# Optimization experiments

Hardware: AMD Instinct MI355X
Metric: run time of the kernel (lower is better)

## Reference

```python
import jax, jax.numpy as jnp
import numpy as np

N_NODES = 50000
NUM_FEATS = 512
HIDDEN = 128
NUM_LAYERS = 4
NUM_CLASSES = 40
N_EDGES = 800000
ALPHA = 0.1
C_MIN = 0.2
RESIDUAL_WEIGHT = C_MIN - ALPHA  # 0.1
BIAS_SRELU = -10.0


def setup_inputs() -> dict:
    key = jax.random.key(0)
    ks = jax.random.split(key, 8)
    x = jax.random.normal(ks[0], (N_NODES, NUM_FEATS), dtype=jnp.float32)
    edge_index = jax.random.randint(ks[1], (2, N_EDGES), 0, N_NODES, dtype=jnp.int64)
    W_in = jax.random.normal(ks[2], (NUM_FEATS, HIDDEN), dtype=jnp.float32) / np.sqrt(NUM_FEATS)
    b_in = jnp.zeros((HIDDEN,), dtype=jnp.float32)
    W_layers = jax.random.normal(ks[3], (NUM_LAYERS, HIDDEN, HIDDEN), dtype=jnp.float32) / np.sqrt(HIDDEN)
    srelu_bias = jnp.full((NUM_LAYERS, HIDDEN), BIAS_SRELU, dtype=jnp.float32)
    W_out = jax.random.normal(ks[4], (HIDDEN, NUM_CLASSES), dtype=jnp.float32) / np.sqrt(HIDDEN)
    b_out = jnp.zeros((NUM_CLASSES,), dtype=jnp.float32)
    return {"x": x, "edge_index": edge_index, "W_in": W_in, "b_in": b_in,
            "W_layers": W_layers, "srelu_bias": srelu_bias,
            "W_out": W_out, "b_out": b_out}


def _gcn_norm(edge_index, n):
    # PyG gcn_norm: add self-loops, symmetric normalization D^-1/2 A D^-1/2
    loop = jnp.arange(n, dtype=edge_index.dtype)
    src = jnp.concatenate([edge_index[0], loop])
    dst = jnp.concatenate([edge_index[1], loop])
    ones = jnp.ones(src.shape[0], dtype=jnp.float32)
    deg = jax.ops.segment_sum(ones, dst, num_segments=n)
    dinv = jnp.where(deg > 0, jax.lax.rsqrt(deg), 0.0)
    norm = dinv[src] * dinv[dst]  # [E+N]
    return src, dst, norm


def reference(x, edge_index, W_in, b_in, W_layers, srelu_bias, W_out, b_out):
    n = x.shape[0]
    src, dst, norm = _gcn_norm(edge_index, n)

    # input layer (eval mode: dropout is identity), non-arxiv path
    h = jax.nn.relu(x @ W_in + b_in)
    x0 = h  # original_x residual anchor

    def layer(h, params):
        W, sb = params
        # sparse gather-scale-scatter aggregation: [E, H] messages
        agg = jax.ops.segment_sum(norm[:, None] * h[src], dst, num_segments=n)
        out = (1.0 - ALPHA - RESIDUAL_WEIGHT) * agg + RESIDUAL_WEIGHT * h + ALPHA * x0
        out = out @ W
        out = jax.nn.relu(out - sb) + sb  # SReLU
        return out, None

    h, _ = jax.lax.scan(layer, h, (W_layers, srelu_bias))
    return h @ W_out + b_out
```

## Files before the change

kernel.cpp:

```cpp
#include <hip/hip_runtime.h>
#include <hip/hip_fp16.h>

#define N_NODES 50000
#define E_EDGES 800000
#define F_IN 512
#define HID 128
#define N_LAYERS 4
#define C_OUT 40
#define SCAN_BLOCKS 196

typedef __attribute__((ext_vector_type(8))) short bf16x8;
typedef __attribute__((ext_vector_type(4))) float f32x4;

#define MFMA16(a, b, c) __builtin_amdgcn_mfma_f32_16x16x32_bf16(a, b, c, 0, 0, 0)

__device__ __forceinline__ void split2(float a, unsigned short& hi, unsigned short& lo) {
    unsigned u = __float_as_uint(a);
    unsigned r = u + 0x7FFFu + ((u >> 16) & 1u);
    hi = (unsigned short)(r >> 16);
    float hf = __uint_as_float(((unsigned)hi) << 16);
    lo = (unsigned short)(__float_as_uint(a - hf) >> 16);
}

__device__ __forceinline__ void async16(void* lds, const void* g) {
    __builtin_amdgcn_global_load_lds(
        (const __attribute__((address_space(1))) unsigned*)g,
        (__attribute__((address_space(3))) unsigned*)lds, 16, 0, 0);
}

__global__ void indeg_count(const int* __restrict__ ei, int* __restrict__ indeg) {
    int e = blockIdx.x * 256 + threadIdx.x;
    if (e < E_EDGES) {
        unsigned d = (unsigned)ei[E_EDGES + e];
        if (d < N_NODES) atomicAdd(&indeg[d], 1);
    }
}

__global__ void scan_p1(const int* __restrict__ indeg, int* __restrict__ bsum,
                        float* __restrict__ dinv) {
    __shared__ int red[4];
    int i = blockIdx.x * 256 + threadIdx.x;
    int v = (i < N_NODES) ? indeg[i] : 0;
    if (i < N_NODES) dinv[i] = rsqrtf(1.0f + (float)v);
    int s = v;
    #pragma unroll
    for (int off = 32; off > 0; off >>= 1) s += __shfl_down(s, off, 64);
    if ((threadIdx.x & 63) == 0) red[threadIdx.x >> 6] = s;
    __syncthreads();
    if (threadIdx.x == 0) bsum[blockIdx.x] = red[0] + red[1] + red[2] + red[3];
}

__launch_bounds__(256)
__global__ void scan_p2(const int* __restrict__ bsum, int* __restrict__ boff,
                        int* __restrict__ rowptr) {
    __shared__ int s[256];
    int t = threadIdx.x;
    int v = (t < SCAN_BLOCKS) ? bsum[t] : 0;
    s[t] = v;
    __syncthreads();
    #pragma unroll
    for (int off = 1; off < 256; off <<= 1) {
        int a = s[t];
        int b = (t >= off) ? s[t - off] : 0;
        __syncthreads();
        s[t] = a + b;
        __syncthreads();
    }
    if (t < SCAN_BLOCKS) boff[t] = (t == 0) ? 0 : s[t - 1];
    if (t == 255) rowptr[N_NODES] = s[SCAN_BLOCKS - 1];
}

__launch_bounds__(256)
__global__ void scan_p3(const int* __restrict__ indeg, const int* __restrict__ boff,
                        int* __restrict__ rowptr, int* __restrict__ cursor) {
    __shared__ int s[256];
    int t = threadIdx.x;
    int i = blockIdx.x * 256 + t;
    int v = (i < N_NODES) ? indeg[i] : 0;
    s[t] = v;
    __syncthreads();
    #pragma unroll
    for (int off = 1; off < 256; off <<= 1) {
        int a = s[t];
        int b = (t >= off) ? s[t - off] : 0;
        __syncthreads();
        s[t] = a + b;
        __syncthreads();
    }
    if (i < N_NODES) {
        int excl = boff[blockIdx.x] + s[t] - v;
        rowptr[i] = excl;
        cursor[i] = excl;
    }
}

__global__ void csr_fill(const int* __restrict__ ei, int* __restrict__ cursor,
                         int* __restrict__ csr) {
    int e = blockIdx.x * 256 + threadIdx.x;
    if (e < E_EDGES) {
        unsigned s = (unsigned)ei[e];
        unsigned d = (unsigned)ei[E_EDGES + e];
        if (s < N_NODES && d < N_NODES) {
            int pos = atomicAdd(&cursor[d], 1);
            csr[pos] = (int)s;
        }
    }
}

__global__ void wprep(const float* __restrict__ Wi, const float* __restrict__ Wl,
                      const float* __restrict__ Wo,
                      unsigned short* __restrict__ Wth, unsigned short* __restrict__ Wtl,
                      unsigned short* __restrict__ Wlth, unsigned short* __restrict__ Wltl,
                      unsigned short* __restrict__ Woth, unsigned short* __restrict__ Wotl) {
    int idx = blockIdx.x * 256 + threadIdx.x;
    unsigned short hi, lo;
    if (idx < F_IN * HID) {
        int k = idx >> 7, n = idx & 127;
        split2(Wi[idx], hi, lo);
        Wth[(size_t)n * F_IN + k] = hi;
        Wtl[(size_t)n * F_IN + k] = lo;
    } else if (idx < 2 * F_IN * HID) {
        int j = idx - F_IN * HID;
        int l = j >> 14, rem = j & 16383;
        int k = rem >> 7, n = rem & 127;
        split2(Wl[j], hi, lo);
        Wlth[(size_t)l * HID * HID + n * HID + k] = hi;
        Wltl[(size_t)l * HID * HID + n * HID + k] = lo;
    } else if (idx < 2 * F_IN * HID + 48 * HID) {
        int j = idx - 2 * F_IN * HID;
        int n = j >> 7, k = j & 127;
        float w = (n < C_OUT) ? Wo[(size_t)k * C_OUT + n] : 0.f;
        split2(w, hi, lo);
        Woth[(size_t)n * HID + k] = hi;
        Wotl[(size_t)n * HID + k] = lo;
    }
}

__launch_bounds__(256)
__global__ void gemm_in_mfma(const float* __restrict__ x,
                             const unsigned short* __restrict__ Bth,
                             const unsigned short* __restrict__ Btl,
                             const float* __restrict__ bi,
                             const float* __restrict__ dinv,
                             float* __restrict__ x0out,
                             __half* __restrict__ g16) {
    __shared__ __align__(16) unsigned short Ah[64 * 32];
    __shared__ __align__(16) unsigned short Al[64 * 32];
    __shared__ __align__(16) unsigned short Bh[2][128 * 32];
    __shared__ __align__(16) unsigned short Bl[2][128 * 32];
    const int t = threadIdx.x;
    const int lane = t & 63;
    const int wv = t >> 6;
    const int wr = wv >> 1, wc = wv & 1;
    const int row0 = blockIdx.x * 64;
    const int fr = lane & 15;
    const int fkg = lane >> 4;
    const float4 z4 = make_float4(0.f, 0.f, 0.f, 0.f);

    f32x4 acc[2][4] = {};

    auto stageB = [&](int buf, int k0) {
        #pragma unroll
        for (int i = 0; i < 2; i++) {
            int g = t + i * 256;
            int n = g >> 2, kg = g & 3;
            int kgp = kg ^ ((n >> 1) & 3);
            size_t src = (size_t)n * F_IN + k0 + kgp * 8;
            async16(&Bh[buf][g * 8], &Bth[src]);
            async16(&Bl[buf][g * 8], &Btl[src]);
        }
    };
    auto loadA = [&](int k0, float4* xr) {
        #pragma unroll
        for (int i = 0; i < 2; i++) {
            int q = t + i * 256;
            int r = q >> 3, c4 = q & 7;
            int grow = row0 + r;
            xr[i] = (grow < N_NODES) ? *(const float4*)&x[(size_t)grow * F_IN + k0 + c4 * 4] : z4;
        }
    };
    auto writeA = [&](const float4* xr) {
        #pragma unroll
        for (int i = 0; i < 2; i++) {
            int q = t + i * 256;
            int r = q >> 3, c4 = q & 7;
            ushort4 uh, ul;
            split2(xr[i].x, uh.x, ul.x); split2(xr[i].y, uh.y, ul.y);
            split2(xr[i].z, uh.z, ul.z); split2(xr[i].w, uh.w, ul.w);
            int gp = (c4 >> 1) ^ ((r >> 1) & 3);
            int idx = r * 32 + gp * 8 + (c4 & 1) * 4;
            *(ushort4*)&Ah[idx] = uh;
            *(ushort4*)&Al[idx] = ul;
        }
    };

    float4 xa[2];
    stageB(0, 0);
    loadA(0, xa);
    writeA(xa);
    __syncthreads();

    int buf = 0;
    for (int step = 0; step < 16; step++) {
        float4 xn[2];
        if (step < 15) {
            stageB(buf ^ 1, (step + 1) * 32);
            loadA((step + 1) * 32, xn);
        }

        int arow0 = wr * 32 + fr;
        bf16x8 ah[2], al[2];
        #pragma unroll
        for (int mt = 0; mt < 2; mt++) {
            int arow = arow0 + mt * 16;
            int aidx = arow * 32 + (fkg ^ ((arow >> 1) & 3)) * 8;
            ah[mt] = *(bf16x8*)&Ah[aidx];
            al[mt] = *(bf16x8*)&Al[aidx];
        }
        #pragma unroll
        for (int nt = 0; nt < 4; nt++) {
            int n = wc * 64 + nt * 16 + fr;
            int bidx = n * 32 + (fkg ^ ((n >> 1) & 3)) * 8;
            bf16x8 bh = *(bf16x8*)&Bh[buf][bidx];
            bf16x8 bl = *(bf16x8*)&Bl[buf][bidx];
            #pragma unroll
            for (int mt = 0; mt < 2; mt++) {
                acc[mt][nt] = MFMA16(al[mt], bh, acc[mt][nt]);
                acc[mt][nt] = MFMA16(ah[mt], bl, acc[mt][nt]);
                acc[mt][nt] = MFMA16(ah[mt], bh, acc[mt][nt]);
            }
        }
        __syncthreads();
        if (step < 15) {
            writeA(xn);
            buf ^= 1;
            __syncthreads();
        }
    }

    const int dcol = lane & 15;
    const int dr0 = (lane >> 4) * 4;
    float dv[2][4];
    #pragma unroll
    for (int mt = 0; mt < 2; mt++)
        #pragma unroll
        for (int j = 0; j < 4; j++) {
            int grow = row0 + wr * 32 + mt * 16 + dr0 + j;
            dv[mt][j] = (grow < N_NODES) ? dinv[grow] : 0.f;
        }
    #pragma unroll
    for (int nt = 0; nt < 4; nt++) {
        int gcol = wc * 64 + nt * 16 + dcol;
        float b = bi[gcol];
        #pragma unroll
        for (int mt = 0; mt < 2; mt++) {
            #pragma unroll
            for (int j = 0; j < 4; j++) {
                int grow = row0 + wr * 32 + mt * 16 + dr0 + j;
                if (grow < N_NODES) {
                    float v = fmaxf(acc[mt][nt][j] + b, 0.f);
                    x0out[(size_t)grow * HID + gcol] = v;
                    g16[(size_t)grow * HID + gcol] = __float2half(dv[mt][j] * v);
                }
            }
        }
    }
}

__launch_bounds__(256)
__global__ void aggregate(const int* __restrict__ rowptr, const int* __restrict__ csr,
                          const float* __restrict__ dinv,
                          const __half* __restrict__ g16,
                          const float* __restrict__ h, const float* __restrict__ x0,
                          float* __restrict__ comb) {
    const int node = blockIdx.x * 4 + (threadIdx.x >> 6);
    const int lane = threadIdx.x & 63;
    if (node >= N_NODES) return;

    const unsigned* g32 = (const unsigned*)g16;
    const float dd = dinv[node];
    const int beg = rowptr[node];
    const int end = rowptr[node + 1];

    float a0 = 0.f, a1 = 0.f, b0 = 0.f, b1 = 0.f;

    #define GACC(r, i) { \
        __half2 p = *(__half2*)&(r); \
        float2 f = __half22float2(p); \
        if ((i) & 1) { b0 += f.x; b1 += f.y; } else { a0 += f.x; a1 += f.y; } }

    int e = beg;
    for (; e + 16 <= end; e += 16) {
        unsigned r[16];
        #pragma unroll
        for (int i = 0; i < 16; i++) r[i] = g32[(size_t)csr[e + i] * 64 + lane];
        #pragma unroll
        for (int i = 0; i < 16; i++) GACC(r[i], i)
    }
    for (; e + 4 <= end; e += 4) {
        unsigned r[4];
        #pragma unroll
        for (int i = 0; i < 4; i++) r[i] = g32[(size_t)csr[e + i] * 64 + lane];
        #pragma unroll
        for (int i = 0; i < 4; i++) GACC(r[i], i)
    }
    for (; e < end; e++) {
        unsigned r = g32[(size_t)csr[e] * 64 + lane];
        GACC(r, 0)
    }
    #undef GACC

    float s0 = a0 + b0, s1 = a1 + b1;
    const float c1 = 0.8f * dd;
    const float c2 = 0.8f * dd * dd + 0.1f;
    float2 hv = ((const float2*)h)[(size_t)node * 64 + lane];
    float2 xv = ((const float2*)x0)[(size_t)node * 64 + lane];
    float2 o;
    o.x = fmaf(c1, s0, fmaf(c2, hv.x, 0.1f * xv.x));
    o.y = fmaf(c1, s1, fmaf(c2, hv.y, 0.1f * xv.y));
    ((float2*)comb)[(size_t)node * 64 + lane] = o;
}

__launch_bounds__(256)
__global__ void gemm_layer_mfma(const unsigned short* __restrict__ Bth,
                                const unsigned short* __restrict__ Btl,
                                const float* __restrict__ sb,
                                const float* __restrict__ dinv,
                                float* __restrict__ comb,
                                __half* __restrict__ g16) {
    __shared__ __align__(16) unsigned short Ah[64 * 128];
    __shared__ __align__(16) unsigned short Al[64 * 128];
    __shared__ __align__(16) unsigned short Bh[128 * 32];
    __shared__ __align__(16) unsigned short Bl[128 * 32];
    const int t = threadIdx.x;
    const int lane = t & 63;
    const int wv = t >> 6;
    const int wr = wv >> 1, wc = wv & 1;
    const int row0 = blockIdx.x * 64;
    const int fr = lane & 15;
    const int fkg = lane >> 4;

    f32x4 acc[2][4] = {};

    auto stageB = [&](int k0) {
        #pragma unroll
        for (int i = 0; i < 2; i++) {
            int g = t + i * 256;
            int n = g >> 2, kg = g & 3;
            int kgp = kg ^ ((n >> 1) & 3);
            size_t src = (size_t)n * HID + k0 + kgp * 8;
            async16(&Bh[g * 8], &Bth[src]);
            async16(&Bl[g * 8], &Btl[src]);
        }
    };

    stageB(0);
    #pragma unroll
    for (int i = 0; i < 8; i++) {
        int q = t + i * 256;
        int r = q >> 5, c4 = q & 31;
        int grow = row0 + r;
        float4 v = make_float4(0.f, 0.f, 0.f, 0.f);
        if (grow < N_NODES) v = *(const float4*)&comb[(size_t)grow * HID + c4 * 4];
        ushort4 uh, ul;
        split2(v.x, uh.x, ul.x); split2(v.y, uh.y, ul.y);
        split2(v.z, uh.z, ul.z); split2(v.w, uh.w, ul.w);
        int idx = (r * 128 + c4 * 4) ^ ((r & 7) << 3);
        *(ushort4*)&Ah[idx] = uh;
        *(ushort4*)&Al[idx] = ul;
    }
    __syncthreads();

    #pragma unroll
    for (int step = 0; step < 4; step++) {
        bf16x8 ah[2], al[2];
        #pragma unroll
        for (int mt = 0; mt < 2; mt++) {
            int arow = wr * 32 + mt * 16 + fr;
            int aidx = (arow * 128 + step * 32 + fkg * 8) ^ ((arow & 7) << 3);
            ah[mt] = *(bf16x8*)&Ah[aidx];
            al[mt] = *(bf16x8*)&Al[aidx];
        }
        #pragma unroll
        for (int nt = 0; nt < 4; nt++) {
            int n = wc * 64 + nt * 16 + fr;
            int bidx = n * 32 + (fkg ^ ((n >> 1) & 3)) * 8;
            bf16x8 bh = *(bf16x8*)&Bh[bidx];
            bf16x8 bl = *(bf16x8*)&Bl[bidx];
            #pragma unroll
            for (int mt = 0; mt < 2; mt++) {
                acc[mt][nt] = MFMA16(al[mt], bh, acc[mt][nt]);
                acc[mt][nt] = MFMA16(ah[mt], bl, acc[mt][nt]);
                acc[mt][nt] = MFMA16(ah[mt], bh, acc[mt][nt]);
            }
        }
        __syncthreads();
        if (step < 3) {
            stageB((step + 1) * 32);
            __syncthreads();
        }
    }

    const int dcol = lane & 15;
    const int dr0 = (lane >> 4) * 4;
    float dv[2][4];
    #pragma unroll
    for (int mt = 0; mt < 2; mt++)
        #pragma unroll
        for (int j = 0; j < 4; j++) {
            int grow = row0 + wr * 32 + mt * 16 + dr0 + j;
            dv[mt][j] = (grow < N_NODES) ? dinv[grow] : 0.f;
        }
    #pragma unroll
    for (int nt = 0; nt < 4; nt++) {
        int gcol = wc * 64 + nt * 16 + dcol;
        float s = sb[gcol];
        #pragma unroll
        for (int mt = 0; mt < 2; mt++) {
            #pragma unroll
            for (int j = 0; j < 4; j++) {
                int grow = row0 + wr * 32 + mt * 16 + dr0 + j;
                if (grow < N_NODES) {
                    float v = fmaxf(acc[mt][nt][j], s);
                    comb[(size_t)grow * HID + gcol] = v;
                    g16[(size_t)grow * HID + gcol] = __float2half(dv[mt][j] * v);
                }
            }
        }
    }
}

__launch_bounds__(256)
__global__ void gemm_layer_out(const unsigned short* __restrict__ Bth,
                               const unsigned short* __restrict__ Btl,
                               const float* __restrict__ sb,
                               const unsigned short* __restrict__ Woth,
                               const unsigned short* __restrict__ Wotl,
                               const float* __restrict__ bo,
                               const float* __restrict__ comb,
                               float* __restrict__ out) {
    __shared__ __align__(16) unsigned short Ah[64 * 128];
    __shared__ __align__(16) unsigned short Al[64 * 128];
    __shared__ __align__(16) unsigned short Bh[128 * 32];
    __shared__ __align__(16) unsigned short Bl[128 * 32];
    const int t = threadIdx.x;
    const int lane = t & 63;
    const int wv = t >> 6;
    const int wr = wv >> 1, wc = wv & 1;
    const int row0 = blockIdx.x * 64;
    const int fr = lane & 15;
    const int fkg = lane >> 4;

    f32x4 acc[2][4] = {};

    auto stageB = [&](int k0) {
        #pragma unroll
        for (int i = 0; i < 2; i++) {
            int g = t + i * 256;
            int n = g >> 2, kg = g & 3;
            int kgp = kg ^ ((n >> 1) & 3);
            size_t src = (size_t)n * HID + k0 + kgp * 8;
            async16(&Bh[g * 8], &Bth[src]);
            async16(&Bl[g * 8], &Btl[src]);
        }
    };

    stageB(0);
    #pragma unroll
    for (int i = 0; i < 8; i++) {
        int q = t + i * 256;
        int r = q >> 5, c4 = q & 31;
        int grow = row0 + r;
        float4 v = make_float4(0.f, 0.f, 0.f, 0.f);
        if (grow < N_NODES) v = *(const float4*)&comb[(size_t)grow * HID + c4 * 4];
        ushort4 uh, ul;
        split2(v.x, uh.x, ul.x); split2(v.y, uh.y, ul.y);
        split2(v.z, uh.z, ul.z); split2(v.w, uh.w, ul.w);
        int idx = (r * 128 + c4 * 4) ^ ((r & 7) << 3);
        *(ushort4*)&Ah[idx] = uh;
        *(ushort4*)&Al[idx] = ul;
    }
    __syncthreads();

    #pragma unroll
    for (int step = 0; step < 4; step++) {
        bf16x8 ah[2], al[2];
        #pragma unroll
        for (int mt = 0; mt < 2; mt++) {
            int arow = wr * 32 + mt * 16 + fr;
            int aidx = (arow * 128 + step * 32 + fkg * 8) ^ ((arow & 7) << 3);
            ah[mt] = *(bf16x8*)&Ah[aidx];
            al[mt] = *(bf16x8*)&Al[aidx];
        }
        #pragma unroll
        for (int nt = 0; nt < 4; nt++) {
            int n = wc * 64 + nt * 16 + fr;
            int bidx = n * 32 + (fkg ^ ((n >> 1) & 3)) * 8;
            bf16x8 bh = *(bf16x8*)&Bh[bidx];
            bf16x8 bl = *(bf16x8*)&Bl[bidx];
            #pragma unroll
            for (int mt = 0; mt < 2; mt++) {
                acc[mt][nt] = MFMA16(al[mt], bh, acc[mt][nt]);
                acc[mt][nt] = MFMA16(ah[mt], bl, acc[mt][nt]);
                acc[mt][nt] = MFMA16(ah[mt], bh, acc[mt][nt]);
            }
        }
        __syncthreads();
        if (step < 3) {
            stageB((step + 1) * 32);
            __syncthreads();
        }
    }

    const int dcol = lane & 15;
    const int dr0 = (lane >> 4) * 4;
    #pragma unroll
    for (int nt = 0; nt < 4; nt++) {
        int col = wc * 64 + nt * 16 + dcol;
        float s = sb[col];
        #pragma unroll
        for (int mt = 0; mt < 2; mt++) {
            #pragma unroll
            for (int j = 0; j < 4; j++) {
                int row = wr * 32 + mt * 16 + dr0 + j;
                float v = fmaxf(acc[mt][nt][j], s);
                unsigned short hi, lo;
                split2(v, hi, lo);
                int idx = (row * 128 + col) ^ ((row & 7) << 3);
                Ah[idx] = hi;
                Al[idx] = lo;
            }
        }
    }
    __syncthreads();

    f32x4 oacc[3] = {};
    #pragma unroll
    for (int kk = 0; kk < 4; kk++) {
        int arow = wv * 16 + fr;
        int aidx = (arow * 128 + kk * 32 + fkg * 8) ^ ((arow & 7) << 3);
        bf16x8 ah = *(bf16x8*)&Ah[aidx];
        bf16x8 al = *(bf16x8*)&Al[aidx];
        #pragma unroll
        for (int nt = 0; nt < 3; nt++) {
            size_t boff = (size_t)(nt * 16 + fr) * HID + kk * 32 + fkg * 8;
            bf16x8 bh = *(const bf16x8*)&Woth[boff];
            bf16x8 bl = *(const bf16x8*)&Wotl[boff];
            oacc[nt] = MFMA16(al, bh, oacc[nt]);
            oacc[nt] = MFMA16(ah, bl, oacc[nt]);
            oacc[nt] = MFMA16(ah, bh, oacc[nt]);
        }
    }
    #pragma unroll
    for (int nt = 0; nt < 3; nt++) {
        int gcol = nt * 16 + dcol;
        if (gcol < C_OUT) {
            float b = bo[gcol];
            #pragma unroll
            for (int j = 0; j < 4; j++) {
                int grow = row0 + wv * 16 + dr0 + j;
                if (grow < N_NODES)
                    out[(size_t)grow * C_OUT + gcol] = oacc[nt][j] + b;
            }
        }
    }
}

extern "C" void kernel_launch(void* const* d_in, const int* in_sizes, int n_in,
                              void* d_out, int out_size, void* d_ws, size_t ws_size,
                              hipStream_t stream) {
    const float* x   = (const float*)d_in[0];
    const int*   ei  = (const int*)d_in[1];
    const float* Wi  = (const float*)d_in[2];
    const float* bi  = (const float*)d_in[3];
    const float* Wls = (const float*)d_in[4];
    const float* sbs = (const float*)d_in[5];
    const float* Wo  = (const float*)d_in[6];
    const float* bo  = (const float*)d_in[7];
    float* out = (float*)d_out;

    float* dinv    = (float*)d_ws;
    int*   indeg   = (int*)(dinv + 50176);
    int*   rowptr  = indeg + 50176;
    int*   cursor  = rowptr + 50304;
    int*   bsum    = cursor + 50176;
    int*   boff    = bsum + 256;
    int*   csr     = boff + 256;
    unsigned short* Wth  = (unsigned short*)(csr + 800000);
    unsigned short* Wtl  = Wth + 65536;
    unsigned short* Wlth = Wtl + 65536;
    unsigned short* Wltl = Wlth + 65536;
    unsigned short* Woth = Wltl + 65536;
    unsigned short* Wotl = Woth + 6144;
    float* x0  = (float*)(Wotl + 6144);
    float* hB  = x0 + (size_t)N_NODES * HID;
    float* hC  = hB + (size_t)N_NODES * HID;
    __half* g16 = (__half*)(hC + (size_t)N_NODES * HID);

    const int edgeBlocks = (E_EDGES + 255) / 256;
    const int gemmBlocks = (N_NODES + 63) / 64;
    const int aggBlocks  = (N_NODES + 3) / 4;
    const int wprepBlocks = (2 * F_IN * HID + 48 * HID + 255) / 256;

    hipMemsetAsync(indeg, 0, N_NODES * sizeof(int), stream);
    indeg_count<<<edgeBlocks, 256, 0, stream>>>(ei, indeg);
    scan_p1<<<SCAN_BLOCKS, 256, 0, stream>>>(indeg, bsum, dinv);
    scan_p2<<<1, 256, 0, stream>>>(bsum, boff, rowptr);
    scan_p3<<<SCAN_BLOCKS, 256, 0, stream>>>(indeg, boff, rowptr, cursor);
    csr_fill<<<edgeBlocks, 256, 0, stream>>>(ei, cursor, csr);
    wprep<<<wprepBlocks, 256, 0, stream>>>(Wi, Wls, Wo, Wth, Wtl, Wlth, Wltl, Woth, Wotl);

    gemm_in_mfma<<<gemmBlocks, 256, 0, stream>>>(x, Wth, Wtl, bi, dinv, x0, g16);

    float* h = x0;
    for (int l = 0; l < N_LAYERS - 1; l++) {
        float* next = (l & 1) ? hC : hB;
        aggregate<<<aggBlocks, 256, 0, stream>>>(rowptr, csr, dinv, g16, h, x0, next);
        gemm_layer_mfma<<<gemmBlocks, 256, 0, stream>>>(Wlth + (size_t)l * HID * HID,
                                                        Wltl + (size_t)l * HID * HID,
                                                        sbs + (size_t)l * HID, dinv,
                                                        next, g16);
        h = next;
    }
    aggregate<<<aggBlocks, 256, 0, stream>>>(rowptr, csr, dinv, g16, h, x0, hC);
    gemm_layer_out<<<gemmBlocks, 256, 0, stream>>>(Wlth + (size_t)3 * HID * HID,
                                                   Wltl + (size_t)3 * HID * HID,
                                                   sbs + (size_t)3 * HID,
                                                   Woth, Wotl, bo, hC, out);
}
```

Baseline: 405.8 us.

## Double-buffer A tile in input GEMM and split edges across half-waves in aggregation

The input GEMM now double-buffers the A tile in LDS and prefetches x two steps ahead. This removes the second per-step barrier and the write-after-compute stall. The aggregation kernel now has each half-wave handle alternate edges with 8-byte loads, so each wave gathers two edges at once, and it combines the halves with a cross-lane shuffle. The aim is more memory-level parallelism for the gather. The cost is extra LDS per block and some lanes idle in the final epilogue.

```diff
diff --git a/kernel.cpp b/kernel.cpp
--- a/kernel.cpp
+++ b/kernel.cpp
@@ -144,8 +144,8 @@
                              const float* __restrict__ dinv,
                              float* __restrict__ x0out,
                              __half* __restrict__ g16) {
-    __shared__ __align__(16) unsigned short Ah[64 * 32];
-    __shared__ __align__(16) unsigned short Al[64 * 32];
+    __shared__ __align__(16) unsigned short Ah[2][64 * 32];
+    __shared__ __align__(16) unsigned short Al[2][64 * 32];
     __shared__ __align__(16) unsigned short Bh[2][128 * 32];
     __shared__ __align__(16) unsigned short Bl[2][128 * 32];
     const int t = threadIdx.x;
@@ -179,7 +179,7 @@
             xr[i] = (grow < N_NODES) ? *(const float4*)&x[(size_t)grow * F_IN + k0 + c4 * 4] : z4;
         }
     };
-    auto writeA = [&](const float4* xr) {
+    auto writeA = [&](int buf, const float4* xr) {
         #pragma unroll
         for (int i = 0; i < 2; i++) {
             int q = t + i * 256;
@@ -189,40 +189,40 @@
             split2(xr[i].z, uh.z, ul.z); split2(xr[i].w, uh.w, ul.w);
             int gp = (c4 >> 1) ^ ((r >> 1) & 3);
             int idx = r * 32 + gp * 8 + (c4 & 1) * 4;
-            *(ushort4*)&Ah[idx] = uh;
-            *(ushort4*)&Al[idx] = ul;
+            *(ushort4*)&Ah[buf][idx] = uh;
+            *(ushort4*)&Al[buf][idx] = ul;
         }
     };
 
-    float4 xa[2];
+    float4 xa[2], xn[2];
+    loadA(0, xa);
     stageB(0, 0);
-    loadA(0, xa);
-    writeA(xa);
+    writeA(0, xa);
+    loadA(32, xa);
     __syncthreads();
 
-    int buf = 0;
+    int cur = 0;
     for (int step = 0; step < 16; step++) {
-        float4 xn[2];
         if (step < 15) {
-            stageB(buf ^ 1, (step + 1) * 32);
-            loadA((step + 1) * 32, xn);
-        }
-
-        int arow0 = wr * 32 + fr;
+            stageB(cur ^ 1, (step + 1) * 32);
+            writeA(cur ^ 1, xa);
+            if (step < 14) loadA((step + 2) * 32, xn);
+        }
+
         bf16x8 ah[2], al[2];
         #pragma unroll
         for (int mt = 0; mt < 2; mt++) {
-            int arow = arow0 + mt * 16;
+            int arow = wr * 32 + mt * 16 + fr;
             int aidx = arow * 32 + (fkg ^ ((arow >> 1) & 3)) * 8;
-            ah[mt] = *(bf16x8*)&Ah[aidx];
-            al[mt] = *(bf16x8*)&Al[aidx];
+            ah[mt] = *(bf16x8*)&Ah[cur][aidx];
+            al[mt] = *(bf16x8*)&Al[cur][aidx];
         }
         #pragma unroll
         for (int nt = 0; nt < 4; nt++) {
             int n = wc * 64 + nt * 16 + fr;
             int bidx = n * 32 + (fkg ^ ((n >> 1) & 3)) * 8;
-            bf16x8 bh = *(bf16x8*)&Bh[buf][bidx];
-            bf16x8 bl = *(bf16x8*)&Bl[buf][bidx];
+            bf16x8 bh = *(bf16x8*)&Bh[cur][bidx];
+            bf16x8 bl = *(bf16x8*)&Bl[cur][bidx];
             #pragma unroll
             for (int mt = 0; mt < 2; mt++) {
                 acc[mt][nt] = MFMA16(al[mt], bh, acc[mt][nt]);
@@ -231,11 +231,8 @@
             }
         }
         __syncthreads();
-        if (step < 15) {
-            writeA(xn);
-            buf ^= 1;
-            __syncthreads();
-        }
+        cur ^= 1;
+        xa[0] = xn[0]; xa[1] = xn[1];
     }
 
     const int dcol = lane & 15;
@@ -277,48 +274,58 @@
     const int lane = threadIdx.x & 63;
     if (node >= N_NODES) return;
 
-    const unsigned* g32 = (const unsigned*)g16;
+    const int half = lane >> 5;
+    const int hl = lane & 31;
+    const unsigned short* gbase = (const unsigned short*)g16;
+
     const float dd = dinv[node];
     const int beg = rowptr[node];
     const int end = rowptr[node + 1];
 
-    float a0 = 0.f, a1 = 0.f, b0 = 0.f, b1 = 0.f;
-
-    #define GACC(r, i) { \
-        __half2 p = *(__half2*)&(r); \
-        float2 f = __half22float2(p); \
-        if ((i) & 1) { b0 += f.x; b1 += f.y; } else { a0 += f.x; a1 += f.y; } }
+    float a0 = 0.f, a1 = 0.f, a2 = 0.f, a3 = 0.f;
+
+    #define ELOAD(ei) (*(const uint2*)(gbase + (size_t)csr[ei] * 128 + hl * 4))
+    #define EACC(r) { \
+        __half2 p0 = *(__half2*)&(r).x, p1 = *(__half2*)&(r).y; \
+        float2 f0 = __half22float2(p0), f1 = __half22float2(p1); \
+        a0 += f0.x; a1 += f0.y; a2 += f1.x; a3 += f1.y; }
 
     int e = beg;
     for (; e + 16 <= end; e += 16) {
-        unsigned r[16];
-        #pragma unroll
-        for (int i = 0; i < 16; i++) r[i] = g32[(size_t)csr[e + i] * 64 + lane];
-        #pragma unroll
-        for (int i = 0; i < 16; i++) GACC(r[i], i)
-    }
-    for (; e + 4 <= end; e += 4) {
-        unsigned r[4];
-        #pragma unroll
-        for (int i = 0; i < 4; i++) r[i] = g32[(size_t)csr[e + i] * 64 + lane];
-        #pragma unroll
-        for (int i = 0; i < 4; i++) GACC(r[i], i)
-    }
-    for (; e < end; e++) {
-        unsigned r = g32[(size_t)csr[e] * 64 + lane];
-        GACC(r, 0)
-    }
-    #undef GACC
-
-    float s0 = a0 + b0, s1 = a1 + b1;
-    const float c1 = 0.8f * dd;
-    const float c2 = 0.8f * dd * dd + 0.1f;
-    float2 hv = ((const float2*)h)[(size_t)node * 64 + lane];
-    float2 xv = ((const float2*)x0)[(size_t)node * 64 + lane];
-    float2 o;
-    o.x = fmaf(c1, s0, fmaf(c2, hv.x, 0.1f * xv.x));
-    o.y = fmaf(c1, s1, fmaf(c2, hv.y, 0.1f * xv.y));
-    ((float2*)comb)[(size_t)node * 64 + lane] = o;
+        uint2 r[8];
+        #pragma unroll
+        for (int i = 0; i < 8; i++) r[i] = ELOAD(e + 2 * i + half);
+        #pragma unroll
+        for (int i = 0; i < 8; i++) EACC(r[i])
+    }
+    for (; e + 2 <= end; e += 2) {
+        uint2 r = ELOAD(e + half);
+        EACC(r)
+    }
+    if (e < end && half == 0) {
+        uint2 r = ELOAD(e);
+        EACC(r)
+    }
+    #undef ELOAD
+    #undef EACC
+
+    a0 += __shfl_xor(a0, 32, 64);
+    a1 += __shfl_xor(a1, 32, 64);
+    a2 += __shfl_xor(a2, 32, 64);
+    a3 += __shfl_xor(a3, 32, 64);
+
+    if (half == 0) {
+        const float c1 = 0.8f * dd;
+        const float c2 = 0.8f * dd * dd + 0.1f;
+        float4 hv = ((const float4*)h)[(size_t)node * 32 + hl];
+        float4 xv = ((const float4*)x0)[(size_t)node * 32 + hl];
+        float4 o;
+        o.x = fmaf(c1, a0, fmaf(c2, hv.x, 0.1f * xv.x));
+        o.y = fmaf(c1, a1, fmaf(c2, hv.y, 0.1f * xv.y));
+        o.z = fmaf(c1, a2, fmaf(c2, hv.z, 0.1f * xv.z));
+        o.w = fmaf(c1, a3, fmaf(c2, hv.w, 0.1f * xv.w));
+        ((float4*)comb)[(size_t)node * 32 + hl] = o;
+    }
 }
 
 __launch_bounds__(256)
```

New measurement: 429.3 us. 1.06x slower.
